# Kernel optimization log

Hardware: AMD Instinct MI355X
Metric: run time of the kernel (lower is better)

The kernel has to match this reference:

```python
import jax, jax.numpy as jnp
from jax import lax
import numpy as np

# ---- init hyperparameters (from init_kwargs) ----
STRIDE = 1
DP_CHANNELS = 1
ATOM_R = 8
ATOM_C = 8
NUMB_ATOM = 128
T_SC = 3
K = 256
BATCH = 32
IMG = 64


def setup_inputs() -> dict:
    key = jax.random.key(0)
    k1, k2 = jax.random.split(key)
    Y = jax.random.normal(k1, (BATCH, DP_CHANNELS, IMG, IMG), dtype=jnp.float32)
    # ConvTranspose2d weight layout: (numb_atom, dp_channels, atom_c, atom_r)
    W = jax.random.normal(k2, (NUMB_ATOM, DP_CHANNELS, ATOM_C, ATOM_R), dtype=jnp.float32)
    # normalise_weights(): each (i, j) filter divided by its L2 norm
    W = W / jnp.sqrt(jnp.sum(W ** 2, axis=(2, 3), keepdims=True))
    return {"Y": Y, "W_D": W}


def _conv_D(X, W):
    # PyTorch ConvTranspose2d (stride=1, no padding): full convolution with
    # spatially-flipped kernel; W is (in=numb_atom, out=dp_channels, kh, kw).
    kh, kw = W.shape[2], W.shape[3]
    return lax.conv_general_dilated(
        X, jnp.flip(W, (2, 3)), (1, 1),
        [(kh - 1, kh - 1), (kw - 1, kw - 1)],
        dimension_numbers=('NCHW', 'IOHW', 'NCHW'))


def _conv_Dt(R, Wt):
    # PyTorch Conv2d (VALID, stride=1): Wt is (out=numb_atom, in=dp, kh, kw)
    return lax.conv_general_dilated(
        R, Wt, (1, 1), 'VALID', dimension_numbers=('NCHW', 'OIHW', 'NCHW'))


def _hard_threshold_k(X, k):
    # keep the k largest-|.| entries per sample (over flattened C,H,W)
    B = X.shape[0]
    flat = X.reshape(B, -1)
    _, idx = lax.top_k(jnp.abs(flat), k)                      # [B, k]
    vals = jnp.take_along_axis(flat, idx, axis=1)             # [B, k]
    out = jnp.zeros_like(flat).at[jnp.arange(B)[:, None], idx].set(vals)
    return out.reshape(X.shape)


def _linesearch(Y, X, W, Wt, k):
    R = Y - _conv_D(X, W)
    g = _conv_Dt(R, Wt)
    l2_start = jnp.sum(R ** 2)

    def attempt(alpha):
        Xu = _hard_threshold_k(X + alpha * g, k)
        err = jnp.sum((Y - _conv_D(Xu, W)) ** 2)
        return Xu, err

    Xu0, err0 = attempt(jnp.float32(1.0))

    def cond(s):
        _, _, err, count = s
        return (err >= l2_start) & (count <= 15)

    def body(s):
        alpha, _, _, count = s
        alpha = alpha * jnp.float32(0.5)
        Xu, err = attempt(alpha)
        return (alpha, Xu, err, count + 1)

    alpha, Xu, err, _ = lax.while_loop(
        cond, body, (jnp.float32(1.0), Xu0, err0, jnp.int32(0)))
    return Xu, err, alpha


def reference(Y, W_D):
    # D_trans.weight = D.weight.permute(0,1,3,2) -> (numb_atom, dp, atom_r, atom_c)
    Wt = jnp.swapaxes(W_D, 2, 3)
    kh, kw = Wt.shape[2], Wt.shape[3]
    B, _, H, W_sp = Y.shape
    X = jnp.zeros((B, W_D.shape[0], H - kh + 1, W_sp - kw + 1), dtype=Y.dtype)
    for _ in range(T_SC):
        X, _, _ = _linesearch(Y, X, W_D, Wt, K)
    return X
```

## Files before the change

kernel.cpp:

```cpp
#include <hip/hip_runtime.h>
#include <stdint.h>

#define NB   32
#define NCH  128
#define IMG  64
#define IMG2 4096
#define OH   57
#define OHW  3249
#define CHW  415872
#define KTOP 256
#define NATT 17
#define NS   32
#define SCAP 512
#define NCAP 1536
#define NBUCK 8192
#define HSHIFT 18
#define TGT  512
#define RSTRIDE 72
#define NZB  257
#define BMW  12996

typedef unsigned long long ull;

__global__ void k_init(int* support_cnt) {
    if (threadIdx.x < NB) support_cnt[threadIdx.x] = 0;
}

__global__ __launch_bounds__(256) void k_resid(
    const float* __restrict__ Y, const float* __restrict__ W,
    const int* __restrict__ support_cnt, const ull* __restrict__ sup_iv,
    float* __restrict__ Rg, double* __restrict__ l2part,
    uint32_t* __restrict__ hist, int* __restrict__ cand_cnt)
{
    int bx = blockIdx.x, tid = threadIdx.x;
    if (bx >= NB) {
        int zb = bx - NB;
        if (zb < 256) {
            ((uint4*)hist)[zb * 256 + tid] = make_uint4(0u, 0u, 0u, 0u);
        } else {
            ((uint4*)cand_cnt)[tid] = make_uint4(0u, 0u, 0u, 0u);
        }
        return;
    }
    int b = bx;
    __shared__ float Rs[IMG2];
    const float4* Y4 = (const float4*)(Y + b * IMG2);
    float4* R4 = (float4*)Rs;
    for (int i = tid; i < IMG2 / 4; i += 256) R4[i] = Y4[i];
    __syncthreads();
    int n = support_cnt[b];
    for (int task = tid; task < n * 64; task += 256) {
        int i = task >> 6, tap = task & 63, p = tap >> 3, q = tap & 7;
        ull iv = sup_iv[b * KTOP + i];
        uint32_t idx = (uint32_t)iv;
        float val = __uint_as_float((uint32_t)(iv >> 32));
        int c = idx / OHW, rem = idx % OHW, s = rem / OH, t = rem % OH;
        float w = W[c * 64 + p * 8 + q];
        atomicAdd(&Rs[(s + p) * IMG + (t + q)], -val * w);
    }
    __syncthreads();
    double acc = 0.0;
    for (int i = tid; i < IMG2; i += 256) {
        float v = Rs[i];
        Rg[b * IMG2 + i] = v;
        acc += (double)v * (double)v;
    }
    __shared__ double red[256];
    red[tid] = acc; __syncthreads();
    for (int s2 = 128; s2 > 0; s2 >>= 1) { if (tid < s2) red[tid] += red[tid + s2]; __syncthreads(); }
    if (tid == 0) l2part[b] = red[0];
}

__global__ __launch_bounds__(256) void k_conv(
    const float* __restrict__ Rg, const float* __restrict__ W,
    float* __restrict__ g_out, uint32_t* __restrict__ hist)
{
    int b = blockIdx.x, cg0 = blockIdx.y, tid = threadIdx.x;
    __shared__ float Rs[71 * 72];
    __shared__ uint32_t hl[NBUCK];
    for (int i = tid; i < 71 * 72; i += 256) Rs[i] = 0.f;
    for (int i = tid; i < NBUCK; i += 256) hl[i] = 0u;
    __syncthreads();
    const float4* R4 = (const float4*)(Rg + b * IMG2);
    for (int i = tid; i < 1024; i += 256) {
        int row = i >> 4, col4 = (i & 15) * 4;
        *(float4*)&Rs[row * 72 + col4] = R4[i];
    }
    __syncthreads();
    int csub = tid >> 7;
    int tile = tid & 127;
    bool active = tile < 120;
    int tr = active ? tile / 15 : 0;
    int tc = active ? tile % 15 : 0;
    int s0 = tr * 8, t0 = tc * 4;

    for (int sub = 0; sub < 4; ++sub) {
        int c = cg0 * 8 + sub * 2 + csub;
        int c_s = __builtin_amdgcn_readfirstlane(c);
        const float* Wc = W + c_s * 64;

        float acc[8][4];
#pragma unroll
        for (int r = 0; r < 8; ++r)
#pragma unroll
            for (int cc = 0; cc < 4; ++cc) acc[r][cc] = 0.f;

#pragma unroll
        for (int rho = 0; rho < 15; ++rho) {
            float rb[12];
            const float* rp = &Rs[(s0 + rho) * 72 + t0];
            *(float4*)&rb[0] = *(const float4*)rp;
            *(float4*)&rb[4] = *(const float4*)(rp + 4);
            *(float4*)&rb[8] = *(const float4*)(rp + 8);
#pragma unroll
            for (int r = 0; r < 8; ++r) {
                const int p = rho - r;
                if (p >= 0 && p < 8) {
#pragma unroll
                    for (int q = 0; q < 8; ++q) {
                        float wv = Wc[q * 8 + p];
#pragma unroll
                        for (int cc = 0; cc < 4; ++cc)
                            acc[r][cc] = fmaf(rb[cc + q], wv, acc[r][cc]);
                    }
                }
            }
        }
        if (active) {
            float* go = g_out + (size_t)(b * NCH + c) * OHW;
#pragma unroll
            for (int r = 0; r < 8; ++r) {
                int s = s0 + r;
                if (s < OH) {
#pragma unroll
                    for (int cc = 0; cc < 4; ++cc) {
                        int t = t0 + cc;
                        if (t < OH) {
                            float v = acc[r][cc];
                            go[s * OH + t] = v;
                            uint32_t bits = __float_as_uint(v) & 0x7fffffffu;
                            atomicAdd(&hl[bits >> HSHIFT], 1u);
                        }
                    }
                }
            }
        }
    }
    __syncthreads();
    for (int i = tid; i < NBUCK; i += 256) {
        uint32_t v = hl[i];
        if (v) atomicAdd(&hist[b * NBUCK + i], v);
    }
}

__global__ __launch_bounds__(256) void k_thresh(const uint32_t* __restrict__ hist,
                                                uint32_t* __restrict__ thr) {
    int b = blockIdx.x, tid = threadIdx.x;
    uint32_t h[32];
    uint32_t s = 0;
    const uint32_t* hb = hist + b * NBUCK + tid * 32;
#pragma unroll
    for (int k = 0; k < 32; ++k) { h[k] = hb[k]; s += h[k]; }
    __shared__ uint32_t buf[2][256];
    int cur = 0;
    buf[0][tid] = s;
    __syncthreads();
    for (int d = 1; d < 256; d <<= 1) {
        uint32_t v = buf[cur][tid];
        if (tid + d < 256) v += buf[cur][tid + d];
        buf[cur ^ 1][tid] = v;
        cur ^= 1;
        __syncthreads();
    }
    uint32_t sufme = buf[cur][tid];
    uint32_t base  = (tid < 255) ? buf[cur][tid + 1] : 0u;
    if (tid == 0 && buf[cur][0] < TGT) thr[b] = 0u;
    if (base < TGT && sufme >= TGT) {
        uint32_t acc = base; int bk = 0;
#pragma unroll
        for (int k = 31; k >= 0; --k) {
            acc += h[k];
            if (acc >= TGT) { bk = tid * 32 + k; break; }
        }
        thr[b] = (uint32_t)bk << HSHIFT;
    }
}

__global__ __launch_bounds__(256) void k_collect(
    const float* __restrict__ g, const uint32_t* __restrict__ thr,
    int* __restrict__ cand_cnt, uint32_t* __restrict__ cand_idx, float* __restrict__ cand_g)
{
    int b = blockIdx.y;
    int i4 = blockIdx.x * 256 + threadIdx.x;
    if (i4 >= CHW / 4) return;
    int slice = blockIdx.x & (NS - 1);
    uint32_t tb = thr[b];
    float4 v4 = ((const float4*)(g + (size_t)b * CHW))[i4];
    float vv[4] = { v4.x, v4.y, v4.z, v4.w };
#pragma unroll
    for (int k = 0; k < 4; ++k) {
        uint32_t bits = __float_as_uint(vv[k]) & 0x7fffffffu;
        if (bits >= tb) {
            int pos = atomicAdd(&cand_cnt[b * NS + slice], 1);
            if (pos < SCAP) {
                cand_idx[(b * NS + slice) * SCAP + pos] = (uint32_t)(i4 * 4 + k);
                cand_g[(b * NS + slice) * SCAP + pos] = vv[k];
            }
        }
    }
}

__global__ __launch_bounds__(1024) void k_suppg(
    const float* __restrict__ g,
    const int* __restrict__ support_cnt, const ull* __restrict__ sup_iv,
    const int* __restrict__ cand_cnt, const uint32_t* __restrict__ cand_idx,
    const float* __restrict__ cand_g,
    uint4* __restrict__ ns_pack, ull* __restrict__ sup_gp, ull* __restrict__ kb_all)
{
    int b = blockIdx.x, tid = threadIdx.x, lane = tid & 63;
    __shared__ uint32_t bm[BMW];
    __shared__ int cnts[NS];
    __shared__ ull ck[NCAP];
    __shared__ float cg_l[NCAP];
    __shared__ int nns_sh;
    int n = support_cnt[b];
    for (int i = tid; i < BMW / 4; i += 1024) ((uint4*)bm)[i] = make_uint4(0u, 0u, 0u, 0u);
    if (tid < NS) cnts[tid] = min(cand_cnt[b * NS + tid], SCAP);
    if (tid == 0) nns_sh = 0;
    __syncthreads();
    if (tid < KTOP) {
        float gv = 0.f, vs = 0.f;
        uint32_t nidx;
        if (tid < n) {
            ull iv = sup_iv[b * KTOP + tid];
            uint32_t idx = (uint32_t)iv;
            nidx = idx;
            vs = __uint_as_float((uint32_t)(iv >> 32));
            atomicOr(&bm[idx >> 5], 1u << (idx & 31));
            gv = g[(size_t)b * CHW + idx];
            int c = idx / OHW, r = idx % OHW, s = r / OH, t = r % OH;
            uint32_t pk = (uint32_t)((c << 12) | (s << 6) | t);
            sup_gp[b * KTOP + tid] = ((ull)__float_as_uint(gv) << 32) | (ull)pk;
        } else {
            nidx = (uint32_t)(CHW + tid);
            sup_gp[b * KTOP + tid] = 0ull;
        }
        ull klo = (ull)(uint32_t)(~nidx);
#pragma unroll
        for (int a2 = 0; a2 < NATT; ++a2) {
            float v2 = (tid < n) ? fmaf(ldexpf(1.f, -a2), gv, vs) : 0.f;
            kb_all[((size_t)a2 * NB + b) * KTOP + tid] =
                ((ull)(__float_as_uint(v2) & 0x7fffffffu) << 32) | klo;
        }
    }
    __syncthreads();
    for (int t0 = tid; t0 < NS * SCAP; t0 += 1024) {
        int s = t0 >> 9, j = t0 & (SCAP - 1);
        bool keep = false; uint32_t idx = 0; float gv = 0.f;
        if (j < cnts[s]) {
            idx = cand_idx[(b * NS + s) * SCAP + j];
            gv = cand_g[(b * NS + s) * SCAP + j];
            keep = ((bm[idx >> 5] >> (idx & 31)) & 1u) == 0u;
        }
        ull mk = __ballot(keep);
        if (mk) {
            int basep = 0;
            if (lane == 0) basep = atomicAdd(&nns_sh, (int)__popcll(mk));
            basep = __shfl(basep, 0, 64);
            if (keep) {
                int p = basep + (int)__popcll(mk & ((1ull << lane) - 1ull));
                if (p < NCAP) {
                    ck[p] = ((ull)(__float_as_uint(gv) & 0x7fffffffu) << 32) | (ull)(uint32_t)(~idx);
                    cg_l[p] = gv;
                }
            }
        }
    }
    __syncthreads();
    int nns = min(nns_sh, NCAP);
    int nns8 = (nns + 7) & ~7;
    for (int i = nns + tid; i < nns8; i += 1024) ck[i] = 0ull;
    __syncthreads();
    ull myk[2]; int myr[2];
#pragma unroll
    for (int q = 0; q < 2; ++q) { int i = tid + 1024 * q; myk[q] = (i < nns) ? ck[i] : 0ull; myr[q] = 0; }
    for (int j = 0; j < nns8; j += 8) {
        ull t0 = ck[j], t1 = ck[j+1], t2 = ck[j+2], t3 = ck[j+3];
        ull t4 = ck[j+4], t5 = ck[j+5], t6 = ck[j+6], t7 = ck[j+7];
#pragma unroll
        for (int q = 0; q < 2; ++q) {
            myr[q] += ((t0 > myk[q]) ? 1 : 0) + ((t1 > myk[q]) ? 1 : 0)
                    + ((t2 > myk[q]) ? 1 : 0) + ((t3 > myk[q]) ? 1 : 0)
                    + ((t4 > myk[q]) ? 1 : 0) + ((t5 > myk[q]) ? 1 : 0)
                    + ((t6 > myk[q]) ? 1 : 0) + ((t7 > myk[q]) ? 1 : 0);
        }
    }
#pragma unroll
    for (int q = 0; q < 2; ++q) {
        int i = tid + 1024 * q;
        if (i < nns && myr[q] < KTOP) {
            uint32_t idx = ~(uint32_t)myk[q];
            int r = myr[q];
            int c = idx / OHW, rr = idx % OHW, s = rr / OH, t = rr % OH;
            uint32_t pk = (uint32_t)((c << 12) | (s << 6) | t);
            ns_pack[b * KTOP + r] = make_uint4(idx, __float_as_uint(cg_l[i]), pk, 0u);
        }
    }
}

__global__ __launch_bounds__(512) void k_att2(
    const float* __restrict__ Y, const float* __restrict__ W,
    const int* __restrict__ support_cnt, const ull* __restrict__ sup_iv,
    const ull* __restrict__ sup_gp, const uint4* __restrict__ ns_pack,
    const ull* __restrict__ kb_all,
    uint32_t* __restrict__ sel_idx, float* __restrict__ sel_val, double* __restrict__ err)
{
    int a = blockIdx.x, b = blockIdx.y, tid = threadIdx.x;
    int lane = tid & 63, wid = tid >> 6;
    float alpha = ldexpf(1.f, -a);
    int n = support_cnt[b];

    __shared__ float recon[64 * RSTRIDE];
    __shared__ ull kA[KTOP];
    __shared__ ull s_pv[KTOP];
    __shared__ uint32_t s_idx[KTOP];
    __shared__ double redd[8];

    uint32_t myi = 0, mypk = 0;
    float myv = 0.f;
    ull myk = 0;
    if (tid < KTOP) {
        uint4 np = ns_pack[b * KTOP + tid];
        myi = np.x;
        myv = alpha * __uint_as_float(np.y);
        mypk = np.z;
        myk = ((ull)(__float_as_uint(myv) & 0x7fffffffu) << 32) | (ull)(uint32_t)(~myi);
        kA[tid] = myk;
    } else {
        int t2 = tid - KTOP;
        ull gp = sup_gp[b * KTOP + t2];
        ull iv = sup_iv[b * KTOP + t2];
        if (t2 < n) {
            myi = (uint32_t)iv;
            myv = fmaf(alpha, __uint_as_float((uint32_t)(gp >> 32)),
                       __uint_as_float((uint32_t)(iv >> 32)));
            mypk = (uint32_t)gp;
        } else {
            myi = (uint32_t)(CHW + t2);
            myv = 0.f; mypk = 0u;
        }
        myk = ((ull)(__float_as_uint(myv) & 0x7fffffffu) << 32) | (ull)(uint32_t)(~myi);
    }

    const float4* Y4 = (const float4*)(Y + b * IMG2);
    float4 y0 = Y4[tid * 2], y1 = Y4[tid * 2 + 1];

    for (int i = tid; i < 64 * RSTRIDE; i += 512) recon[i] = 0.f;
    __syncthreads();

    const ull* __restrict__ kb = kb_all + ((size_t)a * NB + b) * KTOP;
    int cb0 = 0, cb1 = 0;
    for (int j = 0; j < KTOP; j += 8) {
        ull t0 = kb[j],     t1 = kb[j + 1], t2 = kb[j + 2], t3 = kb[j + 3];
        ull t4 = kb[j + 4], t5 = kb[j + 5], t6 = kb[j + 6], t7 = kb[j + 7];
        cb0 += ((t0 > myk) ? 1 : 0) + ((t1 > myk) ? 1 : 0)
             + ((t2 > myk) ? 1 : 0) + ((t3 > myk) ? 1 : 0);
        cb1 += ((t4 > myk) ? 1 : 0) + ((t5 > myk) ? 1 : 0)
             + ((t6 > myk) ? 1 : 0) + ((t7 > myk) ? 1 : 0);
    }
    int cb = cb0 + cb1;
    int rank;
    if (tid < KTOP) {
        rank = tid + cb;
    } else {
        int lo = 0, hi = KTOP;
        while (lo < hi) { int mid = (lo + hi) >> 1; if (kA[mid] > myk) lo = mid + 1; else hi = mid; }
        rank = lo + cb;
    }
    if (rank < KTOP) {
        s_pv[rank] = ((ull)__float_as_uint(myv) << 32) | (ull)mypk;
        s_idx[rank] = myi;
    }
    __syncthreads();

    {
        int p = lane >> 3, q = lane & 7;
        ull pv[4]; float wv[4];
#pragma unroll
        for (int j = 0; j < 4; ++j) pv[j] = s_pv[wid + 8 * j];
#pragma unroll
        for (int j = 0; j < 4; ++j) wv[j] = W[(((uint32_t)pv[j]) >> 12) * 64 + lane];
#pragma unroll
        for (int k4 = 0; k4 < 32; k4 += 4) {
            ull npv[4] = {0, 0, 0, 0}; float nwv[4] = {0.f, 0.f, 0.f, 0.f};
            if (k4 + 4 < 32) {
#pragma unroll
                for (int j = 0; j < 4; ++j) npv[j] = s_pv[wid + 8 * (k4 + 4 + j)];
#pragma unroll
                for (int j = 0; j < 4; ++j) nwv[j] = W[(((uint32_t)npv[j]) >> 12) * 64 + lane];
            }
#pragma unroll
            for (int j = 0; j < 4; ++j) {
                uint32_t pk = (uint32_t)pv[j];
                float val = __uint_as_float((uint32_t)(pv[j] >> 32));
                int s = (pk >> 6) & 63, t = pk & 63;
                atomicAdd(&recon[(s + p) * RSTRIDE + (t + q)], val * wv[j]);
            }
#pragma unroll
            for (int j = 0; j < 4; ++j) { pv[j] = npv[j]; wv[j] = nwv[j]; }
        }
    }
    __syncthreads();

    double accd = 0.0;
    {
        int idx0 = tid * 2;
        const float* rr = &recon[(idx0 >> 4) * RSTRIDE + (idx0 & 15) * 4];
        float d0 = y0.x - rr[0]; accd += (double)d0 * (double)d0;
        float d1 = y0.y - rr[1]; accd += (double)d1 * (double)d1;
        float d2 = y0.z - rr[2]; accd += (double)d2 * (double)d2;
        float d3 = y0.w - rr[3]; accd += (double)d3 * (double)d3;
        int idx1 = tid * 2 + 1;
        rr = &recon[(idx1 >> 4) * RSTRIDE + (idx1 & 15) * 4];
        float e0 = y1.x - rr[0]; accd += (double)e0 * (double)e0;
        float e1 = y1.y - rr[1]; accd += (double)e1 * (double)e1;
        float e2 = y1.z - rr[2]; accd += (double)e2 * (double)e2;
        float e3 = y1.w - rr[3]; accd += (double)e3 * (double)e3;
    }
    for (int d = 32; d > 0; d >>= 1) accd += __shfl_xor(accd, d, 64);
    if (lane == 0) redd[wid] = accd;
    __syncthreads();
    if (tid == 0) {
        double e = 0.0;
#pragma unroll
        for (int w2 = 0; w2 < 8; ++w2) e += redd[w2];
        err[a * NB + b] = e;
    }

    if (tid < KTOP) {
        size_t o = ((size_t)a * NB + b) * KTOP;
        ull pvt = s_pv[tid];
        sel_idx[o + tid] = s_idx[tid];
        sel_val[o + tid] = __uint_as_float((uint32_t)(pvt >> 32));
    }
}

__global__ __launch_bounds__(256) void k_update(
    const double* __restrict__ l2part, const double* __restrict__ err,
    const uint32_t* __restrict__ sel_idx, const float* __restrict__ sel_val,
    int* __restrict__ support_cnt, ull* __restrict__ sup_iv)
{
    int b = blockIdx.x, tid = threadIdx.x;
    __shared__ double esum[NATT + 1];
    __shared__ int sel_sh;
    if (tid < NATT) {
        double e = 0.0;
        for (int b2 = 0; b2 < NB; ++b2) e += err[tid * NB + b2];
        esum[tid] = e;
    } else if (tid == NATT) {
        double l2 = 0.0;
        for (int b2 = 0; b2 < NB; ++b2) l2 += l2part[b2];
        esum[NATT] = l2;
    }
    __syncthreads();
    if (tid == 0) {
        double l2 = esum[NATT];
        int sel = NATT - 1;
        for (int a2 = 0; a2 < NATT; ++a2) if (esum[a2] < l2) { sel = a2; break; }
        sel_sh = sel;
    }
    __syncthreads();
    int a = sel_sh;
    __shared__ uint32_t ki[KTOP];
    __shared__ float kv[KTOP];
    ki[tid] = sel_idx[((size_t)a * NB + b) * KTOP + tid];
    kv[tid] = sel_val[((size_t)a * NB + b) * KTOP + tid];
    __syncthreads();
    uint32_t me = ki[tid];
    int rank = 0;
    for (int j = 0; j < KTOP; j += 8) {
        uint32_t a0 = ki[j], a1 = ki[j+1], a2 = ki[j+2], a3 = ki[j+3];
        uint32_t a4 = ki[j+4], a5 = ki[j+5], a6 = ki[j+6], a7 = ki[j+7];
        rank += ((a0 < me) ? 1 : 0) + ((a1 < me) ? 1 : 0) + ((a2 < me) ? 1 : 0) + ((a3 < me) ? 1 : 0)
              + ((a4 < me) ? 1 : 0) + ((a5 < me) ? 1 : 0) + ((a6 < me) ? 1 : 0) + ((a7 < me) ? 1 : 0);
    }
    sup_iv[b * KTOP + rank] = (ull)me | ((ull)__float_as_uint(kv[tid]) << 32);
    if (tid == 0) support_cnt[b] = KTOP;
}

__global__ void k_outzero(float4* __restrict__ out) {
    int i = blockIdx.x * 256 + threadIdx.x;
    if (i < (NB * CHW) / 4) out[i] = make_float4(0.f, 0.f, 0.f, 0.f);
}

__global__ void k_scatter(const ull* __restrict__ sup_iv, float* __restrict__ out) {
    int b = blockIdx.x, tid = threadIdx.x;
    if (tid < KTOP) {
        ull iv = sup_iv[b * KTOP + tid];
        out[(size_t)b * CHW + (uint32_t)iv] = __uint_as_float((uint32_t)(iv >> 32));
    }
}

static size_t align256(size_t x) { return (x + 255) & ~(size_t)255; }

extern "C" void kernel_launch(void* const* d_in, const int* in_sizes, int n_in,
                              void* d_out, int out_size, void* d_ws, size_t ws_size,
                              hipStream_t stream)
{
    const float* Y = (const float*)d_in[0];
    const float* W = (const float*)d_in[1];
    float* out = (float*)d_out;

    char* p = (char*)d_ws;
    size_t off = 0;
    auto carve = [&](size_t bytes) { void* r = p + off; off = align256(off + bytes); return r; };
    float*    Rg          = (float*)   carve(NB * IMG2 * sizeof(float));
    uint32_t* hist        = (uint32_t*)carve((size_t)NB * NBUCK * sizeof(uint32_t));
    uint32_t* thr         = (uint32_t*)carve(NB * sizeof(uint32_t));
    int*      cand_cnt    = (int*)     carve(NB * NS * sizeof(int));
    double*   l2part      = (double*)  carve(NB * sizeof(double));
    double*   err         = (double*)  carve(NATT * NB * sizeof(double));
    int*      support_cnt = (int*)     carve(NB * sizeof(int));
    ull*      sup_iv      = (ull*)     carve((size_t)NB * KTOP * sizeof(ull));
    uint32_t* sel_idx     = (uint32_t*)carve((size_t)NATT * NB * KTOP * sizeof(uint32_t));
    float*    sel_val     = (float*)   carve((size_t)NATT * NB * KTOP * sizeof(float));
    uint32_t* cand_idx    = (uint32_t*)carve((size_t)NB * NS * SCAP * sizeof(uint32_t));
    float*    cand_g      = (float*)   carve((size_t)NB * NS * SCAP * sizeof(float));
    uint4*    ns_pack     = (uint4*)   carve((size_t)NB * KTOP * sizeof(uint4));
    ull*      sup_gp      = (ull*)     carve((size_t)NB * KTOP * sizeof(ull));
    ull*      kb_all      = (ull*)     carve((size_t)NATT * NB * KTOP * sizeof(ull));
    (void)ws_size; (void)in_sizes; (void)n_in; (void)out_size;

    k_init<<<1, 64, 0, stream>>>(support_cnt);
    for (int t = 0; t < 3; ++t) {
        k_resid<<<NB + NZB, 256, 0, stream>>>(Y, W, support_cnt, sup_iv,
                                              Rg, l2part, hist, cand_cnt);
        k_conv<<<dim3(NB, 16), 256, 0, stream>>>(Rg, W, out, hist);
        k_thresh<<<NB, 256, 0, stream>>>(hist, thr);
        k_collect<<<dim3((CHW / 4 + 255) / 256, NB), 256, 0, stream>>>(out, thr, cand_cnt, cand_idx, cand_g);
        k_suppg<<<NB, 1024, 0, stream>>>(out, support_cnt, sup_iv,
                                         cand_cnt, cand_idx, cand_g,
                                         ns_pack, sup_gp, kb_all);
        k_att2<<<dim3(NATT, NB), 512, 0, stream>>>(Y, W, support_cnt, sup_iv,
                                                   sup_gp, ns_pack, kb_all,
                                                   sel_idx, sel_val, err);
        k_update<<<NB, 256, 0, stream>>>(l2part, err, sel_idx, sel_val,
                                         support_cnt, sup_iv);
    }
    k_outzero<<<((NB * CHW) / 4 + 255) / 256, 256, 0, stream>>>((float4*)out);
    k_scatter<<<NB, 256, 0, stream>>>(sup_iv, out);
}
```

Baseline: 662.4 us.

## Fold threshold and support-update kernels into conv and residual kernels

The per-iteration histogram threshold computation moves into k_conv: the last of the 16 channel-group blocks for each batch is elected through an atomic done-counter and computes the threshold. The line-search selection and support update, formerly in k_update, now happen at the start of k_resid and in a new final scatter kernel, with l2 partials double-buffered across iterations. This removes two launches per iteration and their global round-trips. In exchange the support list is no longer sorted by index, which later kernels might rely on, and there is an extra fence and atomic per block.

```diff
diff --git a/kernel.cpp b/kernel.cpp
--- a/kernel.cpp
+++ b/kernel.cpp
@@ -28,9 +28,11 @@
 
 __global__ __launch_bounds__(256) void k_resid(
     const float* __restrict__ Y, const float* __restrict__ W,
-    const int* __restrict__ support_cnt, const ull* __restrict__ sup_iv,
-    float* __restrict__ Rg, double* __restrict__ l2part,
-    uint32_t* __restrict__ hist, int* __restrict__ cand_cnt)
+    const double* __restrict__ l2prev, const double* __restrict__ errv,
+    const uint32_t* __restrict__ sel_idx, const float* __restrict__ sel_val, int t,
+    int* __restrict__ support_cnt, ull* __restrict__ sup_iv,
+    float* __restrict__ Rg, double* __restrict__ l2cur,
+    uint32_t* __restrict__ hist, int* __restrict__ zero_arena)
 {
     int bx = blockIdx.x, tid = threadIdx.x;
     if (bx >= NB) {
@@ -38,25 +40,62 @@
         if (zb < 256) {
             ((uint4*)hist)[zb * 256 + tid] = make_uint4(0u, 0u, 0u, 0u);
         } else {
-            ((uint4*)cand_cnt)[tid] = make_uint4(0u, 0u, 0u, 0u);
+            ((uint4*)zero_arena)[tid] = make_uint4(0u, 0u, 0u, 0u);
+            ((uint4*)zero_arena)[tid + 256] = make_uint4(0u, 0u, 0u, 0u);
         }
         return;
     }
     int b = bx;
     __shared__ float Rs[IMG2];
+    __shared__ uint32_t s_si[KTOP];
+    __shared__ float s_sv[KTOP];
+    __shared__ double red[256];
+    __shared__ int a_sh;
+
     const float4* Y4 = (const float4*)(Y + b * IMG2);
     float4* R4 = (float4*)Rs;
     for (int i = tid; i < IMG2 / 4; i += 256) R4[i] = Y4[i];
-    __syncthreads();
-    int n = support_cnt[b];
+
+    int n = 0;
+    if (t > 0) {
+        if (tid < NATT) {
+            double e = 0.0;
+#pragma unroll 8
+            for (int b2 = 0; b2 < NB; ++b2) e += errv[tid * NB + b2];
+            red[tid] = e;
+        } else if (tid == NATT) {
+            double l2 = 0.0;
+#pragma unroll 8
+            for (int b2 = 0; b2 < NB; ++b2) l2 += l2prev[b2];
+            red[NATT] = l2;
+        }
+        __syncthreads();
+        if (tid == 0) {
+            double l2 = red[NATT];
+            int sel = NATT - 1;
+            for (int a2 = 0; a2 < NATT; ++a2) if (red[a2] < l2) { sel = a2; break; }
+            a_sh = sel;
+        }
+        __syncthreads();
+        int a = a_sh;
+        size_t o = ((size_t)a * NB + b) * KTOP;
+        uint32_t mi = sel_idx[o + tid];
+        float mv = sel_val[o + tid];
+        s_si[tid] = mi;
+        s_sv[tid] = mv;
+        sup_iv[b * KTOP + tid] = (ull)mi | ((ull)__float_as_uint(mv) << 32);
+        if (tid == 0) support_cnt[b] = KTOP;
+        n = KTOP;
+    }
+    __syncthreads();
+
     for (int task = tid; task < n * 64; task += 256) {
         int i = task >> 6, tap = task & 63, p = tap >> 3, q = tap & 7;
-        ull iv = sup_iv[b * KTOP + i];
-        uint32_t idx = (uint32_t)iv;
-        float val = __uint_as_float((uint32_t)(iv >> 32));
-        int c = idx / OHW, rem = idx % OHW, s = rem / OH, t = rem % OH;
+        uint32_t idx = s_si[i];
+        float val = s_sv[i];
+        int c = idx / OHW, rem = idx % OHW, s = rem / OH, tt = rem % OH;
         float w = W[c * 64 + p * 8 + q];
-        atomicAdd(&Rs[(s + p) * IMG + (t + q)], -val * w);
+        atomicAdd(&Rs[(s + p) * IMG + (tt + q)], -val * w);
     }
     __syncthreads();
     double acc = 0.0;
@@ -65,19 +104,20 @@
         Rg[b * IMG2 + i] = v;
         acc += (double)v * (double)v;
     }
-    __shared__ double red[256];
     red[tid] = acc; __syncthreads();
     for (int s2 = 128; s2 > 0; s2 >>= 1) { if (tid < s2) red[tid] += red[tid + s2]; __syncthreads(); }
-    if (tid == 0) l2part[b] = red[0];
+    if (tid == 0) l2cur[b] = red[0];
 }
 
 __global__ __launch_bounds__(256) void k_conv(
     const float* __restrict__ Rg, const float* __restrict__ W,
-    float* __restrict__ g_out, uint32_t* __restrict__ hist)
+    float* __restrict__ g_out, uint32_t* __restrict__ hist,
+    int* __restrict__ done_cnt, uint32_t* __restrict__ thr)
 {
     int b = blockIdx.x, cg0 = blockIdx.y, tid = threadIdx.x;
     __shared__ float Rs[71 * 72];
     __shared__ uint32_t hl[NBUCK];
+    __shared__ int elect_sh;
     for (int i = tid; i < 71 * 72; i += 256) Rs[i] = 0.f;
     for (int i = tid; i < NBUCK; i += 256) hl[i] = 0u;
     __syncthreads();
@@ -151,38 +191,49 @@
         uint32_t v = hl[i];
         if (v) atomicAdd(&hist[b * NBUCK + i], v);
     }
-}
-
-__global__ __launch_bounds__(256) void k_thresh(const uint32_t* __restrict__ hist,
-                                                uint32_t* __restrict__ thr) {
-    int b = blockIdx.x, tid = threadIdx.x;
-    uint32_t h[32];
-    uint32_t s = 0;
-    const uint32_t* hb = hist + b * NBUCK + tid * 32;
-#pragma unroll
-    for (int k = 0; k < 32; ++k) { h[k] = hb[k]; s += h[k]; }
-    __shared__ uint32_t buf[2][256];
-    int cur = 0;
-    buf[0][tid] = s;
-    __syncthreads();
-    for (int d = 1; d < 256; d <<= 1) {
-        uint32_t v = buf[cur][tid];
-        if (tid + d < 256) v += buf[cur][tid + d];
-        buf[cur ^ 1][tid] = v;
-        cur ^= 1;
+    __syncthreads();
+    if (tid == 0) {
+        __threadfence();
+        int old = atomicAdd(&done_cnt[b], 1);
+        elect_sh = (old == 15) ? 1 : 0;
+    }
+    __syncthreads();
+    if (elect_sh) {
+        uint32_t h[32];
+        uint32_t s = 0;
+        const uint32_t* hb = hist + b * NBUCK + tid * 32;
+#pragma unroll
+        for (int k = 0; k < 32; ++k) {
+            h[k] = __hip_atomic_load(&hb[k], __ATOMIC_RELAXED, __HIP_MEMORY_SCOPE_AGENT);
+            s += h[k];
+        }
+        uint32_t* buf0 = hl;
+        uint32_t* buf1 = hl + 256;
+        int cur = 0;
+        buf0[tid] = s;
         __syncthreads();
-    }
-    uint32_t sufme = buf[cur][tid];
-    uint32_t base  = (tid < 255) ? buf[cur][tid + 1] : 0u;
-    if (tid == 0 && buf[cur][0] < TGT) thr[b] = 0u;
-    if (base < TGT && sufme >= TGT) {
-        uint32_t acc = base; int bk = 0;
-#pragma unroll
-        for (int k = 31; k >= 0; --k) {
-            acc += h[k];
-            if (acc >= TGT) { bk = tid * 32 + k; break; }
-        }
-        thr[b] = (uint32_t)bk << HSHIFT;
+        for (int d = 1; d < 256; d <<= 1) {
+            uint32_t* bc = cur ? buf1 : buf0;
+            uint32_t* bn = cur ? buf0 : buf1;
+            uint32_t v = bc[tid];
+            if (tid + d < 256) v += bc[tid + d];
+            bn[tid] = v;
+            cur ^= 1;
+            __syncthreads();
+        }
+        uint32_t* bc = cur ? buf1 : buf0;
+        uint32_t sufme = bc[tid];
+        uint32_t base  = (tid < 255) ? bc[tid + 1] : 0u;
+        if (tid == 0 && bc[0] < TGT) thr[b] = 0u;
+        if (base < TGT && sufme >= TGT) {
+            uint32_t acc2 = base; int bk = 0;
+#pragma unroll
+            for (int k = 31; k >= 0; --k) {
+                acc2 += h[k];
+                if (acc2 >= TGT) { bk = tid * 32 + k; break; }
+            }
+            thr[b] = (uint32_t)bk << HSHIFT;
+        }
     }
 }
 
@@ -445,60 +496,40 @@
     }
 }
 
-__global__ __launch_bounds__(256) void k_update(
-    const double* __restrict__ l2part, const double* __restrict__ err,
-    const uint32_t* __restrict__ sel_idx, const float* __restrict__ sel_val,
-    int* __restrict__ support_cnt, ull* __restrict__ sup_iv)
-{
-    int b = blockIdx.x, tid = threadIdx.x;
-    __shared__ double esum[NATT + 1];
-    __shared__ int sel_sh;
-    if (tid < NATT) {
-        double e = 0.0;
-        for (int b2 = 0; b2 < NB; ++b2) e += err[tid * NB + b2];
-        esum[tid] = e;
-    } else if (tid == NATT) {
-        double l2 = 0.0;
-        for (int b2 = 0; b2 < NB; ++b2) l2 += l2part[b2];
-        esum[NATT] = l2;
-    }
-    __syncthreads();
-    if (tid == 0) {
-        double l2 = esum[NATT];
-        int sel = NATT - 1;
-        for (int a2 = 0; a2 < NATT; ++a2) if (esum[a2] < l2) { sel = a2; break; }
-        sel_sh = sel;
-    }
-    __syncthreads();
-    int a = sel_sh;
-    __shared__ uint32_t ki[KTOP];
-    __shared__ float kv[KTOP];
-    ki[tid] = sel_idx[((size_t)a * NB + b) * KTOP + tid];
-    kv[tid] = sel_val[((size_t)a * NB + b) * KTOP + tid];
-    __syncthreads();
-    uint32_t me = ki[tid];
-    int rank = 0;
-    for (int j = 0; j < KTOP; j += 8) {
-        uint32_t a0 = ki[j], a1 = ki[j+1], a2 = ki[j+2], a3 = ki[j+3];
-        uint32_t a4 = ki[j+4], a5 = ki[j+5], a6 = ki[j+6], a7 = ki[j+7];
-        rank += ((a0 < me) ? 1 : 0) + ((a1 < me) ? 1 : 0) + ((a2 < me) ? 1 : 0) + ((a3 < me) ? 1 : 0)
-              + ((a4 < me) ? 1 : 0) + ((a5 < me) ? 1 : 0) + ((a6 < me) ? 1 : 0) + ((a7 < me) ? 1 : 0);
-    }
-    sup_iv[b * KTOP + rank] = (ull)me | ((ull)__float_as_uint(kv[tid]) << 32);
-    if (tid == 0) support_cnt[b] = KTOP;
-}
-
 __global__ void k_outzero(float4* __restrict__ out) {
     int i = blockIdx.x * 256 + threadIdx.x;
     if (i < (NB * CHW) / 4) out[i] = make_float4(0.f, 0.f, 0.f, 0.f);
 }
 
-__global__ void k_scatter(const ull* __restrict__ sup_iv, float* __restrict__ out) {
+__global__ __launch_bounds__(256) void k_scatter2(
+    const double* __restrict__ l2f, const double* __restrict__ errv,
+    const uint32_t* __restrict__ sel_idx, const float* __restrict__ sel_val,
+    float* __restrict__ out)
+{
     int b = blockIdx.x, tid = threadIdx.x;
-    if (tid < KTOP) {
-        ull iv = sup_iv[b * KTOP + tid];
-        out[(size_t)b * CHW + (uint32_t)iv] = __uint_as_float((uint32_t)(iv >> 32));
-    }
+    __shared__ double red2[NATT + 1];
+    __shared__ int a_sh;
+    if (tid < NATT) {
+        double e = 0.0;
+#pragma unroll 8
+        for (int b2 = 0; b2 < NB; ++b2) e += errv[tid * NB + b2];
+        red2[tid] = e;
+    } else if (tid == NATT) {
+        double l2 = 0.0;
+#pragma unroll 8
+        for (int b2 = 0; b2 < NB; ++b2) l2 += l2f[b2];
+        red2[NATT] = l2;
+    }
+    __syncthreads();
+    if (tid == 0) {
+        double l2 = red2[NATT];
+        int sel = NATT - 1;
+        for (int a2 = 0; a2 < NATT; ++a2) if (red2[a2] < l2) { sel = a2; break; }
+        a_sh = sel;
+    }
+    __syncthreads();
+    size_t o = ((size_t)a_sh * NB + b) * KTOP;
+    out[(size_t)b * CHW + sel_idx[o + tid]] = sel_val[o + tid];
 }
 
 static size_t align256(size_t x) { return (x + 255) & ~(size_t)255; }
@@ -517,9 +548,9 @@
     float*    Rg          = (float*)   carve(NB * IMG2 * sizeof(float));
     uint32_t* hist        = (uint32_t*)carve((size_t)NB * NBUCK * sizeof(uint32_t));
     uint32_t* thr         = (uint32_t*)carve(NB * sizeof(uint32_t));
-    int*      cand_cnt    = (int*)     carve(NB * NS * sizeof(int));
-    double*   l2part      = (double*)  carve(NB * sizeof(double));
-    double*   err         = (double*)  carve(NATT * NB * sizeof(double));
+    int*      zero_arena  = (int*)     carve(8192 * sizeof(int));
+    double*   l2part      = (double*)  carve(2 * NB * sizeof(double));
+    double*   err         = (double*)  carve((size_t)NATT * NB * sizeof(double));
     int*      support_cnt = (int*)     carve(NB * sizeof(int));
     ull*      sup_iv      = (ull*)     carve((size_t)NB * KTOP * sizeof(ull));
     uint32_t* sel_idx     = (uint32_t*)carve((size_t)NATT * NB * KTOP * sizeof(uint32_t));
@@ -531,12 +562,16 @@
     ull*      kb_all      = (ull*)     carve((size_t)NATT * NB * KTOP * sizeof(ull));
     (void)ws_size; (void)in_sizes; (void)n_in; (void)out_size;
 
+    int*      cand_cnt    = zero_arena;
+    int*      done_cnt    = zero_arena + 1024;
+
     k_init<<<1, 64, 0, stream>>>(support_cnt);
     for (int t = 0; t < 3; ++t) {
-        k_resid<<<NB + NZB, 256, 0, stream>>>(Y, W, support_cnt, sup_iv,
-                                              Rg, l2part, hist, cand_cnt);
-        k_conv<<<dim3(NB, 16), 256, 0, stream>>>(Rg, W, out, hist);
-        k_thresh<<<NB, 256, 0, stream>>>(hist, thr);
+        double* l2cur  = l2part + (t & 1) * NB;
+        double* l2prev = l2part + ((t + 1) & 1) * NB;
+        k_resid<<<NB + NZB, 256, 0, stream>>>(Y, W, l2prev, err, sel_idx, sel_val, t,
+                                              support_cnt, sup_iv, Rg, l2cur, hist, zero_arena);
+        k_conv<<<dim3(NB, 16), 256, 0, stream>>>(Rg, W, out, hist, done_cnt, thr);
         k_collect<<<dim3((CHW / 4 + 255) / 256, NB), 256, 0, stream>>>(out, thr, cand_cnt, cand_idx, cand_g);
         k_suppg<<<NB, 1024, 0, stream>>>(out, support_cnt, sup_iv,
                                          cand_cnt, cand_idx, cand_g,
@@ -544,9 +579,7 @@
         k_att2<<<dim3(NATT, NB), 512, 0, stream>>>(Y, W, support_cnt, sup_iv,
                                                    sup_gp, ns_pack, kb_all,
                                                    sel_idx, sel_val, err);
-        k_update<<<NB, 256, 0, stream>>>(l2part, err, sel_idx, sel_val,
-                                         support_cnt, sup_iv);
     }
     k_outzero<<<((NB * CHW) / 4 + 255) / 256, 256, 0, stream>>>((float4*)out);
-    k_scatter<<<NB, 256, 0, stream>>>(sup_iv, out);
-}
+    k_scatter2<<<NB, 256, 0, stream>>>(l2part, err, sel_idx, sel_val, out);
+}
```

After: 699.2 us. 5.6% more time.
